# Kernel optimization log

Measured on AMD Instinct MI355X. Metric: run time of the kernel, lower is better.

The kernel has to match this reference:

```python
import jax, jax.numpy as jnp
import numpy as np

HIDDEN = 1024
HEADS = 16
HEAD_DIM = HIDDEN // HEADS
EPS = 1e-5


def setup_inputs() -> dict:
    key = jax.random.key(0)
    ks = jax.random.split(key, 9)
    B, S, H = 2, 2048, HIDDEN
    scale = 1.0 / np.sqrt(H)
    inp = {
        "hidden_states": jax.random.normal(ks[0], (B, S, H), dtype=jnp.float32),
        "Wq": jax.random.normal(ks[1], (H, H), dtype=jnp.float32) * scale,
        "bq": jnp.zeros((H,), jnp.float32),
        "Wk": jax.random.normal(ks[2], (H, H), dtype=jnp.float32) * scale,
        "bk": jnp.zeros((H,), jnp.float32),
        "Wv": jax.random.normal(ks[3], (H, H), dtype=jnp.float32) * scale,
        "bv": jnp.zeros((H,), jnp.float32),
        "Wo": jax.random.normal(ks[4], (H, H), dtype=jnp.float32) * scale,
        "bo": jnp.zeros((H,), jnp.float32),
        "gamma": jnp.ones((H,), jnp.float32),
        "beta": jnp.zeros((H,), jnp.float32),
    }
    return inp


def reference(hidden_states, Wq, bq, Wk, bk, Wv, bv, Wo, bo, gamma, beta):
    B, S, H = hidden_states.shape
    residual = hidden_states

    def shape(x):  # [B,S,H] -> [B,heads,S,head_dim]
        return x.reshape(B, S, HEADS, HEAD_DIM).transpose(0, 2, 1, 3)

    q = shape(hidden_states @ Wq + bq)
    k = shape(hidden_states @ Wk + bk)
    v = shape(hidden_states @ Wv + bv)

    scores = jnp.einsum("bhqd,bhkd->bhqk", q, k) / jnp.sqrt(
        jnp.asarray(HEAD_DIM, hidden_states.dtype))
    probs = jax.nn.softmax(scores, axis=-1)
    context = jnp.einsum("bhqk,bhkd->bhqd", probs, v)
    context = context.transpose(0, 2, 1, 3).reshape(B, S, H)

    output = context @ Wo + bo
    x = output + residual
    mu = jnp.mean(x, axis=-1, keepdims=True)
    var = jnp.mean(jnp.square(x - mu), axis=-1, keepdims=True)
    return (x - mu) * jax.lax.rsqrt(var + EPS) * gamma + beta
```

## Files before the change

kernel.cpp:

```cpp
#include <hip/hip_runtime.h>
#include <hip/hip_bf16.h>
#include <math.h>

#define HIDDEN 1024
#define HEADS 16
#define HEAD_DIM 64
#define EPS 1e-5f

typedef __attribute__((ext_vector_type(8))) short bf16x8;
typedef __attribute__((ext_vector_type(4))) float f32x4;

#if defined(__has_builtin)
#if __has_builtin(__builtin_amdgcn_exp2f)
#define EXP2(x) __builtin_amdgcn_exp2f(x)
#endif
#endif
#ifndef EXP2
#define EXP2(x) exp2f(x)
#endif

#define QSCALE 0.18033688011112042f

__device__ __forceinline__ short f2bf(float f) {
    union { float f; unsigned u; } v; v.f = f;
    unsigned r = v.u + 0x7fffu + ((v.u >> 16) & 1u);
    return (short)(r >> 16);
}

__device__ __forceinline__ void gl_lds16(const void* g, void* l) {
    __builtin_amdgcn_global_load_lds(
        (const __attribute__((address_space(1))) void*)g,
        (__attribute__((address_space(3))) void*)l, 16, 0, 0);
}

__global__ __launch_bounds__(256) void prep_kernel(
    const float* __restrict__ X,
    const float* __restrict__ Wq, const float* __restrict__ Wk,
    const float* __restrict__ Wv, const float* __restrict__ Wo,
    const float* __restrict__ bq, const float* __restrict__ bk,
    const float* __restrict__ bv,
    short* __restrict__ Xb, short* __restrict__ Wt3, short* __restrict__ Wot,
    float* __restrict__ b3)
{
    __shared__ short tile[32][33];
    const int id = blockIdx.x;
    if (id < 4096) {
        int i = id * 1024 + threadIdx.x * 4;
        float4 v = *(const float4*)(X + i);
        short o[4] = { f2bf(v.x), f2bf(v.y), f2bf(v.z), f2bf(v.w) };
        *(uint2*)(Xb + i) = *(uint2*)o;
    } else if (id < 8192) {
        int t = id - 4096;
        const int wsel = t >> 10; t &= 1023;
        const float* W = (wsel == 0) ? Wq : (wsel == 1) ? Wk : (wsel == 2) ? Wv : Wo;
        short* dst = (wsel < 3) ? (Wt3 + (size_t)wsel * 1024 * 1024) : Wot;
        const float scale = (wsel == 0) ? QSCALE : 1.0f;
        int n0 = (t & 31) * 32;
        int k0 = (t >> 5) * 32;
        int tx = threadIdx.x & 31;
        int ty = threadIdx.x >> 5;
        #pragma unroll
        for (int i = 0; i < 32; i += 8)
            tile[ty + i][tx] = f2bf(W[(size_t)(k0 + ty + i) * 1024 + n0 + tx] * scale);
        __syncthreads();
        #pragma unroll
        for (int i = 0; i < 32; i += 8)
            dst[(size_t)(n0 + ty + i) * 1024 + k0 + tx] = tile[tx][ty + i];
    } else {
        int i = (id - 8192) * 256 + threadIdx.x;
        if (i < 3072) {
            float v = (i < 1024) ? bq[i] * QSCALE
                    : (i < 2048) ? bk[i - 1024] : bv[i - 2048];
            b3[i] = v;
        }
    }
}

__global__ __launch_bounds__(256) void gemm_bt_mfma(
    const short* __restrict__ A, const short* __restrict__ Bt,
    const float* __restrict__ bias,
    void* __restrict__ C0, int ldc0,
    void* __restrict__ C1, int split_col, int ldc1,
    const float* __restrict__ resid,
    int M, int N, int K, int out_bf16)
{
    __shared__ short As[128 * 32];
    __shared__ short Bs[128 * 32];
    const int tid = threadIdx.x;
    const int wave = tid >> 6, lane = tid & 63;
    const int ln16 = lane & 15, quad = lane >> 4;
    const int wm = (wave >> 1) * 64, wn = (wave & 1) * 64;
    const int brow = blockIdx.y * 128, bcol = blockIdx.x * 128;

    const int sr  = lane >> 2;
    const int scb = lane & 3;

    f32x4 acc[4][4];
    #pragma unroll
    for (int mt = 0; mt < 4; ++mt)
        #pragma unroll
        for (int nt = 0; nt < 4; ++nt) acc[mt][nt] = (f32x4){0.f, 0.f, 0.f, 0.f};

    for (int k0 = 0; k0 < K; k0 += 32) {
        __syncthreads();
        #pragma unroll
        for (int i = 0; i < 2; ++i) {
            int rb = i * 64 + wave * 16;
            int r  = rb + sr;
            int csrc = (scb ^ ((r >> 1) & 3)) * 8;
            gl_lds16(A  + (size_t)(brow + r) * K + k0 + csrc, &As[rb * 32]);
            gl_lds16(Bt + (size_t)(bcol + r) * K + k0 + csrc, &Bs[rb * 32]);
        }
        __syncthreads();

        bf16x8 af[4], bf[4];
        #pragma unroll
        for (int mt = 0; mt < 4; ++mt) {
            int r = wm + mt * 16 + ln16;
            af[mt] = *(const bf16x8*)&As[r * 32 + ((quad ^ ((r >> 1) & 3)) * 8)];
        }
        #pragma unroll
        for (int nt = 0; nt < 4; ++nt) {
            int r = wn + nt * 16 + ln16;
            bf[nt] = *(const bf16x8*)&Bs[r * 32 + ((quad ^ ((r >> 1) & 3)) * 8)];
        }
        #pragma unroll
        for (int mt = 0; mt < 4; ++mt)
            #pragma unroll
            for (int nt = 0; nt < 4; ++nt)
                acc[mt][nt] = __builtin_amdgcn_mfma_f32_16x16x32_bf16(
                    af[mt], bf[nt], acc[mt][nt], 0, 0, 0);
    }

    void* Cp = C0; int ld = ldc0; int coff = 0;
    if (bcol >= split_col) { Cp = C1; ld = ldc1; coff = split_col; }

    #pragma unroll
    for (int mt = 0; mt < 4; ++mt) {
        #pragma unroll
        for (int r = 0; r < 4; ++r) {
            int row = brow + wm + mt * 16 + quad * 4 + r;
            #pragma unroll
            for (int nt = 0; nt < 4; ++nt) {
                int col = bcol + wn + nt * 16 + ln16;
                float v = acc[mt][nt][r] + bias[col];
                if (resid) v += resid[(size_t)row * N + col];
                if (out_bf16) ((short*)Cp)[(size_t)row * ld + (col - coff)] = f2bf(v);
                else          ((float*)Cp)[(size_t)row * ld + (col - coff)] = v;
            }
        }
    }
}

__global__ __launch_bounds__(256) void vtranspose_kernel(
    const short* __restrict__ Vb, short* __restrict__ VT)
{
    __shared__ short t[64][72];
    const int c0 = blockIdx.x * 64;
    const int r0 = blockIdx.y * 64;
    const int tid = threadIdx.x;
    #pragma unroll
    for (int i = 0; i < 2; ++i) {
        int idx = tid + i * 256;
        int r = idx >> 3, cc = (idx & 7) * 8;
        *(uint4*)&t[r][cc] = *(const uint4*)(Vb + (size_t)(r0 + r) * 1024 + c0 + cc);
    }
    __syncthreads();
    #pragma unroll
    for (int i = 0; i < 2; ++i) {
        int idx = tid + i * 256;
        int c = idx >> 3, rr = (idx & 7) * 8;
        short tmp[8];
        #pragma unroll
        for (int j = 0; j < 8; ++j) tmp[j] = t[rr + j][c];
        *(uint4*)(VT + (size_t)(c0 + c) * 4096 + r0 + rr) = *(uint4*)tmp;
    }
}

__global__ __launch_bounds__(128) void attn_mfma_kernel(
    const short* __restrict__ QKb, const short* __restrict__ VT,
    short* __restrict__ Ctx)
{
    const int S = 2048;
    const int h = blockIdx.x, qt = blockIdx.y, b = blockIdx.z;
    const int tid = threadIdx.x;
    const int wave = tid >> 6, lane = tid & 63;
    const int ln16 = lane & 15, quad = lane >> 4;

    __shared__ short Ks[64 * 64];
    __shared__ short Vs[64 * 64];
    __shared__ short Ps[128 * 72];

    const int q0 = qt * 128 + wave * 64;

    bf16x8 qfrag[4][2];
    #pragma unroll
    for (int qg = 0; qg < 4; ++qg)
        #pragma unroll
        for (int kb = 0; kb < 2; ++kb)
            qfrag[qg][kb] = *(const bf16x8*)(QKb +
                (size_t)(b * S + q0 + qg * 16 + ln16) * 2048 + h * 64 + kb * 32 + quad * 8);

    bf16x8 ones;
    #pragma unroll
    for (int j = 0; j < 8; ++j) ones[j] = (short)0x3F80;

    f32x4 of[4][4], lacc[4];
    #pragma unroll
    for (int qg = 0; qg < 4; ++qg) {
        lacc[qg] = (f32x4){0.f, 0.f, 0.f, 0.f};
        #pragma unroll
        for (int nt = 0; nt < 4; ++nt) of[qg][nt] = (f32x4){0.f, 0.f, 0.f, 0.f};
    }

    const int sr  = lane >> 3;
    const int scb = lane & 7;

    for (int kt = 0; kt < S / 64; ++kt) {
        __syncthreads();
        #pragma unroll
        for (int i = 0; i < 4; ++i) {
            int ci = wave * 4 + i;
            int r  = ci * 8 + sr;
            int csrc = ((scb ^ (r & 7))) * 8;
            gl_lds16(QKb + (size_t)(b * S + kt * 64 + r) * 2048 + 1024 + h * 64 + csrc,
                     &Ks[ci * 512]);
            gl_lds16(VT + (size_t)(h * 64 + r) * 4096 + b * S + kt * 64 + csrc,
                     &Vs[ci * 512]);
        }
        __syncthreads();

        #pragma unroll
        for (int nt = 0; nt < 4; ++nt) {
            bf16x8 kf[2];
            #pragma unroll
            for (int kb = 0; kb < 2; ++kb) {
                int r = nt * 16 + ln16;
                int cb = (kb * 4 + quad) ^ (r & 7);
                kf[kb] = *(const bf16x8*)&Ks[r * 64 + cb * 8];
            }
            #pragma unroll
            for (int qg = 0; qg < 4; ++qg) {
                f32x4 a = (f32x4){0.f, 0.f, 0.f, 0.f};
                a = __builtin_amdgcn_mfma_f32_16x16x32_bf16(kf[0], qfrag[qg][0], a, 0, 0, 0);
                a = __builtin_amdgcn_mfma_f32_16x16x32_bf16(kf[1], qfrag[qg][1], a, 0, 0, 0);
                float p0 = EXP2(a[0]), p1 = EXP2(a[1]);
                float p2 = EXP2(a[2]), p3 = EXP2(a[3]);
                union { __hip_bfloat162 h2; unsigned u; } c01, c23;
                c01.h2 = __float22bfloat162_rn(make_float2(p0, p1));
                c23.h2 = __float22bfloat162_rn(make_float2(p2, p3));
                uint2 w; w.x = c01.u; w.y = c23.u;
                *(uint2*)&Ps[(wave * 64 + qg * 16 + ln16) * 72 + nt * 16 + quad * 4] = w;
            }
        }

        bf16x8 pf[4][2];
        #pragma unroll
        for (int qg = 0; qg < 4; ++qg)
            #pragma unroll
            for (int kb = 0; kb < 2; ++kb)
                pf[qg][kb] = *(const bf16x8*)
                    &Ps[(wave * 64 + qg * 16 + ln16) * 72 + kb * 32 + quad * 8];

        #pragma unroll
        for (int qg = 0; qg < 4; ++qg) {
            lacc[qg] = __builtin_amdgcn_mfma_f32_16x16x32_bf16(pf[qg][0], ones, lacc[qg], 0, 0, 0);
            lacc[qg] = __builtin_amdgcn_mfma_f32_16x16x32_bf16(pf[qg][1], ones, lacc[qg], 0, 0, 0);
        }
        #pragma unroll
        for (int nt = 0; nt < 4; ++nt) {
            bf16x8 vf[2];
            #pragma unroll
            for (int kb = 0; kb < 2; ++kb) {
                int r = nt * 16 + ln16;
                int cb = (kb * 4 + quad) ^ (r & 7);
                vf[kb] = *(const bf16x8*)&Vs[r * 64 + cb * 8];
            }
            #pragma unroll
            for (int qg = 0; qg < 4; ++qg) {
                of[qg][nt] = __builtin_amdgcn_mfma_f32_16x16x32_bf16(pf[qg][0], vf[0], of[qg][nt], 0, 0, 0);
                of[qg][nt] = __builtin_amdgcn_mfma_f32_16x16x32_bf16(pf[qg][1], vf[1], of[qg][nt], 0, 0, 0);
            }
        }
    }

    #pragma unroll
    for (int qg = 0; qg < 4; ++qg) {
        #pragma unroll
        for (int r = 0; r < 4; ++r) {
            float inv = 1.f / lacc[qg][r];
            int row = b * S + q0 + qg * 16 + quad * 4 + r;
            #pragma unroll
            for (int nt = 0; nt < 4; ++nt)
                Ctx[(size_t)row * 1024 + h * 64 + nt * 16 + ln16] =
                    f2bf(of[qg][nt][r] * inv);
        }
    }
}

__global__ __launch_bounds__(256) void resln_kernel(
    const float* __restrict__ xin, const float* __restrict__ gamma,
    const float* __restrict__ beta, float* __restrict__ out)
{
    const int row = blockIdx.x;
    const int tid = threadIdx.x;
    const int wid = tid >> 6, lane = tid & 63;
    __shared__ float red[8];

    float4 x = *(const float4*)(xin + (size_t)row * HIDDEN + tid * 4);
    float s = x.x + x.y + x.z + x.w;
    #pragma unroll
    for (int off = 32; off > 0; off >>= 1) s += __shfl_xor(s, off, 64);
    if (lane == 0) red[wid] = s;
    __syncthreads();
    float mu = (red[0] + red[1] + red[2] + red[3]) * (1.f / HIDDEN);

    float dx = x.x - mu, dy = x.y - mu, dz = x.z - mu, dw = x.w - mu;
    float v = dx * dx + dy * dy + dz * dz + dw * dw;
    #pragma unroll
    for (int off = 32; off > 0; off >>= 1) v += __shfl_xor(v, off, 64);
    if (lane == 0) red[4 + wid] = v;
    __syncthreads();
    float var = (red[4] + red[5] + red[6] + red[7]) * (1.f / HIDDEN);
    float rstd = rsqrtf(var + EPS);

    float4 g = *(const float4*)(gamma + tid * 4);
    float4 bt = *(const float4*)(beta + tid * 4);
    float4 o;
    o.x = dx * rstd * g.x + bt.x;
    o.y = dy * rstd * g.y + bt.y;
    o.z = dz * rstd * g.z + bt.z;
    o.w = dw * rstd * g.w + bt.w;
    *(float4*)(out + (size_t)row * HIDDEN + tid * 4) = o;
}

extern "C" void kernel_launch(void* const* d_in, const int* in_sizes, int n_in,
                              void* d_out, int out_size, void* d_ws, size_t ws_size,
                              hipStream_t stream)
{
    const float* X     = (const float*)d_in[0];
    const float* Wq    = (const float*)d_in[1];
    const float* bq    = (const float*)d_in[2];
    const float* Wk    = (const float*)d_in[3];
    const float* bk    = (const float*)d_in[4];
    const float* Wv    = (const float*)d_in[5];
    const float* bv    = (const float*)d_in[6];
    const float* Wo    = (const float*)d_in[7];
    const float* bo    = (const float*)d_in[8];
    const float* gamma = (const float*)d_in[9];
    const float* beta  = (const float*)d_in[10];
    float* out = (float*)d_out;

    const int B = 2, S = 2048;
    const int M = B * S;
    const size_t mat = (size_t)M * HIDDEN;

    char* ws = (char*)d_ws;
    short* Xb  = (short*)(ws);
    short* VT  = (short*)(ws);
    short* Wot = (short*)(ws + (8ull << 20));
    short* Wt3 = (short*)(ws + (10ull << 20));
    float* b3  = (float*)(ws + (16ull << 20));
    short* QKb = (short*)(ws + (17ull << 20));
    float* Pj  = (float*)(ws + (17ull << 20));
    short* Vb  = (short*)(ws + (33ull << 20));
    short* Ctx = (short*)(ws + (33ull << 20));

    dim3 blk(256);

    prep_kernel<<<dim3(8204), blk, 0, stream>>>(X, Wq, Wk, Wv, Wo, bq, bk, bv,
                                                Xb, Wt3, Wot, b3);

    dim3 qkvgrid(3072 / 128, M / 128);
    gemm_bt_mfma<<<qkvgrid, blk, 0, stream>>>(Xb, Wt3, b3,
                                              QKb, 2048, Vb, 2048, 1024,
                                              nullptr, M, 3072, HIDDEN, 1);

    vtranspose_kernel<<<dim3(16, 64), blk, 0, stream>>>(Vb, VT);

    dim3 agrid(HEADS, S / 128, B);
    attn_mfma_kernel<<<agrid, dim3(128), 0, stream>>>(QKb, VT, Ctx);

    dim3 ogrid(HIDDEN / 128, M / 128);
    gemm_bt_mfma<<<ogrid, blk, 0, stream>>>(Ctx, Wot, bo,
                                            Pj, 1024, nullptr, 1 << 30, 0,
                                            X, M, HIDDEN, HIDDEN, 0);

    resln_kernel<<<M, blk, 0, stream>>>(Pj, gamma, beta, out);
}
```

Measured before the change: 257.1 us.

## Fuse V transpose into QKV GEMM epilogue and split attention KV across waves

The QKV GEMM epilogue now writes the V columns directly in transposed layout, which removes the separate vtranspose kernel and its round trip through memory. The attention kernel moves to 256 threads: two wave pairs each handle half of the key tiles for the same 64 queries, and their partial outputs and row sums are combined through shared memory at the end. This doubles the waves per block and the parallelism along the KV axis, at the cost of more LDS and a final reduction. The transposed V stores are 8-byte scattered writes, which may be less efficient than coalesced ones.

Measured after the change: 248.0 us. -3.6%, faster.

```diff
diff --git a/kernel.cpp b/kernel.cpp
--- a/kernel.cpp
+++ b/kernel.cpp
@@ -80,7 +80,7 @@
     const short* __restrict__ A, const short* __restrict__ Bt,
     const float* __restrict__ bias,
     void* __restrict__ C0, int ldc0,
-    void* __restrict__ C1, int split_col, int ldc1,
+    void* __restrict__ C1, int split_col, int ldc1, int v_transpose,
     const float* __restrict__ resid,
     int M, int N, int K, int out_bf16)
 {
@@ -132,6 +132,24 @@
                     af[mt], bf[nt], acc[mt][nt], 0, 0, 0);
     }
 
+    if (v_transpose && bcol >= split_col) {
+        #pragma unroll
+        for (int mt = 0; mt < 4; ++mt) {
+            int row0 = brow + wm + mt * 16 + quad * 4;
+            #pragma unroll
+            for (int nt = 0; nt < 4; ++nt) {
+                int col = bcol + wn + nt * 16 + ln16;
+                int feat = col - split_col;
+                float bz = bias[col];
+                short pk[4];
+                #pragma unroll
+                for (int r = 0; r < 4; ++r) pk[r] = f2bf(acc[mt][nt][r] + bz);
+                *(uint2*)((short*)C1 + (size_t)feat * ldc1 + row0) = *(uint2*)pk;
+            }
+        }
+        return;
+    }
+
     void* Cp = C0; int ld = ldc0; int coff = 0;
     if (bcol >= split_col) { Cp = C1; ld = ldc1; coff = split_col; }
 
@@ -152,32 +170,7 @@
     }
 }
 
-__global__ __launch_bounds__(256) void vtranspose_kernel(
-    const short* __restrict__ Vb, short* __restrict__ VT)
-{
-    __shared__ short t[64][72];
-    const int c0 = blockIdx.x * 64;
-    const int r0 = blockIdx.y * 64;
-    const int tid = threadIdx.x;
-    #pragma unroll
-    for (int i = 0; i < 2; ++i) {
-        int idx = tid + i * 256;
-        int r = idx >> 3, cc = (idx & 7) * 8;
-        *(uint4*)&t[r][cc] = *(const uint4*)(Vb + (size_t)(r0 + r) * 1024 + c0 + cc);
-    }
-    __syncthreads();
-    #pragma unroll
-    for (int i = 0; i < 2; ++i) {
-        int idx = tid + i * 256;
-        int c = idx >> 3, rr = (idx & 7) * 8;
-        short tmp[8];
-        #pragma unroll
-        for (int j = 0; j < 8; ++j) tmp[j] = t[rr + j][c];
-        *(uint4*)(VT + (size_t)(c0 + c) * 4096 + r0 + rr) = *(uint4*)tmp;
-    }
-}
-
-__global__ __launch_bounds__(128) void attn_mfma_kernel(
+__global__ __launch_bounds__(256) void attn_mfma_kernel(
     const short* __restrict__ QKb, const short* __restrict__ VT,
     short* __restrict__ Ctx)
 {
@@ -186,20 +179,21 @@
     const int tid = threadIdx.x;
     const int wave = tid >> 6, lane = tid & 63;
     const int ln16 = lane & 15, quad = lane >> 4;
-
-    __shared__ short Ks[64 * 64];
-    __shared__ short Vs[64 * 64];
-    __shared__ short Ps[128 * 72];
-
-    const int q0 = qt * 128 + wave * 64;
-
+    const int qh = wave >> 1, kh = wave & 1;
+
+    __shared__ short Ks[2][64 * 64];
+    __shared__ short Vs[2][64 * 64];
+    __shared__ short Ps[256 * 72];
+    __shared__ float Ls[128];
+
+    const int qbase = b * S + qt * 128 + qh * 64;
     bf16x8 qfrag[4][2];
     #pragma unroll
     for (int qg = 0; qg < 4; ++qg)
         #pragma unroll
         for (int kb = 0; kb < 2; ++kb)
             qfrag[qg][kb] = *(const bf16x8*)(QKb +
-                (size_t)(b * S + q0 + qg * 16 + ln16) * 2048 + h * 64 + kb * 32 + quad * 8);
+                (size_t)(qbase + qg * 16 + ln16) * 2048 + h * 64 + kb * 32 + quad * 8);
 
     bf16x8 ones;
     #pragma unroll
@@ -213,20 +207,27 @@
         for (int nt = 0; nt < 4; ++nt) of[qg][nt] = (f32x4){0.f, 0.f, 0.f, 0.f};
     }
 
+    const int st  = wave >> 1;
+    const int skv = wave & 1;
     const int sr  = lane >> 3;
     const int scb = lane & 7;
 
-    for (int kt = 0; kt < S / 64; ++kt) {
+    for (int p = 0; p < 16; ++p) {
         __syncthreads();
         #pragma unroll
-        for (int i = 0; i < 4; ++i) {
-            int ci = wave * 4 + i;
-            int r  = ci * 8 + sr;
-            int csrc = ((scb ^ (r & 7))) * 8;
-            gl_lds16(QKb + (size_t)(b * S + kt * 64 + r) * 2048 + 1024 + h * 64 + csrc,
-                     &Ks[ci * 512]);
-            gl_lds16(VT + (size_t)(h * 64 + r) * 4096 + b * S + kt * 64 + csrc,
-                     &Vs[ci * 512]);
+        for (int c = 0; c < 8; ++c) {
+            int r = c * 8 + sr;
+            int csrc = (scb ^ (r & 7)) * 8;
+            int ktp = 2 * p + st;
+            if (skv == 0) {
+                gl_lds16(QKb + (size_t)(b * S + ktp * 64 + r) * 2048
+                             + 1024 + h * 64 + csrc,
+                         &Ks[st][c * 512]);
+            } else {
+                gl_lds16(VT + (size_t)(h * 64 + r) * 4096
+                            + b * S + ktp * 64 + csrc,
+                         &Vs[st][c * 512]);
+            }
         }
         __syncthreads();
 
@@ -237,7 +238,7 @@
             for (int kb = 0; kb < 2; ++kb) {
                 int r = nt * 16 + ln16;
                 int cb = (kb * 4 + quad) ^ (r & 7);
-                kf[kb] = *(const bf16x8*)&Ks[r * 64 + cb * 8];
+                kf[kb] = *(const bf16x8*)&Ks[kh][r * 64 + cb * 8];
             }
             #pragma unroll
             for (int qg = 0; qg < 4; ++qg) {
@@ -274,7 +275,7 @@
             for (int kb = 0; kb < 2; ++kb) {
                 int r = nt * 16 + ln16;
                 int cb = (kb * 4 + quad) ^ (r & 7);
-                vf[kb] = *(const bf16x8*)&Vs[r * 64 + cb * 8];
+                vf[kb] = *(const bf16x8*)&Vs[kh][r * 64 + cb * 8];
             }
             #pragma unroll
             for (int qg = 0; qg < 4; ++qg) {
@@ -284,16 +285,37 @@
         }
     }
 
-    #pragma unroll
-    for (int qg = 0; qg < 4; ++qg) {
-        #pragma unroll
-        for (int r = 0; r < 4; ++r) {
-            float inv = 1.f / lacc[qg][r];
-            int row = b * S + q0 + qg * 16 + quad * 4 + r;
-            #pragma unroll
-            for (int nt = 0; nt < 4; ++nt)
-                Ctx[(size_t)row * 1024 + h * 64 + nt * 16 + ln16] =
-                    f2bf(of[qg][nt][r] * inv);
+    float* Os = (float*)Ps;
+    float* OsQ = Os + qh * (64 * 66);
+    __syncthreads();
+    if (kh == 1) {
+        #pragma unroll
+        for (int qg = 0; qg < 4; ++qg) {
+            #pragma unroll
+            for (int r = 0; r < 4; ++r) {
+                int ql = qg * 16 + quad * 4 + r;
+                #pragma unroll
+                for (int nt = 0; nt < 4; ++nt)
+                    OsQ[ql * 66 + nt * 16 + ln16] = of[qg][nt][r];
+                if (ln16 == 0) Ls[qh * 64 + ql] = lacc[qg][r];
+            }
+        }
+    }
+    __syncthreads();
+    if (kh == 0) {
+        #pragma unroll
+        for (int qg = 0; qg < 4; ++qg) {
+            #pragma unroll
+            for (int r = 0; r < 4; ++r) {
+                int ql = qg * 16 + quad * 4 + r;
+                float inv = 1.f / (lacc[qg][r] + Ls[qh * 64 + ql]);
+                int row = qbase + ql;
+                #pragma unroll
+                for (int nt = 0; nt < 4; ++nt) {
+                    float v = of[qg][nt][r] + OsQ[ql * 66 + nt * 16 + ln16];
+                    Ctx[(size_t)row * 1024 + h * 64 + nt * 16 + ln16] = f2bf(v * inv);
+                }
+            }
         }
     }
 }
@@ -353,18 +375,16 @@
 
     const int B = 2, S = 2048;
     const int M = B * S;
-    const size_t mat = (size_t)M * HIDDEN;
 
     char* ws = (char*)d_ws;
     short* Xb  = (short*)(ws);
-    short* VT  = (short*)(ws);
     short* Wot = (short*)(ws + (8ull << 20));
     short* Wt3 = (short*)(ws + (10ull << 20));
     float* b3  = (float*)(ws + (16ull << 20));
     short* QKb = (short*)(ws + (17ull << 20));
     float* Pj  = (float*)(ws + (17ull << 20));
-    short* Vb  = (short*)(ws + (33ull << 20));
-    short* Ctx = (short*)(ws + (33ull << 20));
+    short* VT  = (short*)(ws + (33ull << 20));
+    short* Ctx = (short*)(ws + (41ull << 20));
 
     dim3 blk(256);
 
@@ -373,17 +393,15 @@
 
     dim3 qkvgrid(3072 / 128, M / 128);
     gemm_bt_mfma<<<qkvgrid, blk, 0, stream>>>(Xb, Wt3, b3,
-                                              QKb, 2048, Vb, 2048, 1024,
+                                              QKb, 2048, VT, 2048, 4096, 1,
                                               nullptr, M, 3072, HIDDEN, 1);
 
-    vtranspose_kernel<<<dim3(16, 64), blk, 0, stream>>>(Vb, VT);
-
     dim3 agrid(HEADS, S / 128, B);
-    attn_mfma_kernel<<<agrid, dim3(128), 0, stream>>>(QKb, VT, Ctx);
+    attn_mfma_kernel<<<agrid, blk, 0, stream>>>(QKb, VT, Ctx);
 
     dim3 ogrid(HIDDEN / 128, M / 128);
     gemm_bt_mfma<<<ogrid, blk, 0, stream>>>(Ctx, Wot, bo,
-                                            Pj, 1024, nullptr, 1 << 30, 0,
+                                            Pj, 1024, nullptr, 1 << 30, 0, 0,
                                             X, M, HIDDEN, HIDDEN, 0);
 
     resln_kernel<<<M, blk, 0, stream>>>(Pj, gamma, beta, out);
```
